# Optimization experiments

Hardware: AMD Instinct MI355X
Metric: run time of the kernel (lower is better)

The kernel has to match this reference:

```python
import jax, jax.numpy as jnp
import numpy as np
from jax.ops import segment_sum

N_NODES = 50000
N_EDGES = 800000
HIDDEN = 96
N_CLASSES = 10
N_GRAPHS = 64


def gcn_conv(x, W, b, src, dst, num_nodes):
    """PyG GCNConv: symmetric-normalized aggregation with self-loops.
    out = D^{-1/2} (A + I) D^{-1/2} (x W) + b, with D the degree of A + I.
    Self-loop contribution handled analytically instead of appending edges.
    """
    ones = jnp.ones((src.shape[0],), dtype=x.dtype)
    deg = segment_sum(ones, dst, num_segments=num_nodes) + 1.0  # +1 for self-loop
    dinv = jax.lax.rsqrt(deg)
    h = x @ W  # [N, H] small GEMM
    norm = dinv[src] * dinv[dst]  # [E]
    msg = h[src] * norm[:, None]  # [E, H] dominant gather
    out = segment_sum(msg, dst, num_segments=num_nodes)  # scatter-add
    out = out + h * (dinv * dinv)[:, None]  # self-loop term
    return out + b


def setup_inputs() -> dict:
    key = jax.random.key(0)
    ks = jax.random.split(key, 12)
    x = jax.random.normal(ks[0], (N_NODES, HIDDEN), dtype=jnp.float32)
    edge_index = jax.random.randint(ks[1], (2, N_EDGES), 0, N_NODES, dtype=jnp.int64)
    batch = jnp.sort(jax.random.randint(ks[2], (N_NODES,), 0, N_GRAPHS, dtype=jnp.int64))
    s = 1.0 / np.sqrt(HIDDEN)
    W0 = jax.random.normal(ks[3], (HIDDEN, HIDDEN), dtype=jnp.float32) * s
    b0 = jnp.zeros((HIDDEN,), dtype=jnp.float32)
    W1 = jax.random.normal(ks[4], (HIDDEN, HIDDEN), dtype=jnp.float32) * s
    b1 = jnp.zeros((HIDDEN,), dtype=jnp.float32)
    W2 = jax.random.normal(ks[5], (HIDDEN, HIDDEN), dtype=jnp.float32) * s
    b2 = jnp.zeros((HIDDEN,), dtype=jnp.float32)
    W_lin = jax.random.normal(ks[6], (HIDDEN, N_CLASSES), dtype=jnp.float32) * s
    b_lin = jnp.zeros((N_CLASSES,), dtype=jnp.float32)
    return {"x": x, "edge_index": edge_index, "batch": batch,
            "W0": W0, "b0": b0, "W1": W1, "b1": b1, "W2": W2, "b2": b2,
            "W_lin": W_lin, "b_lin": b_lin}


def reference(x, edge_index, batch, W0, b0, W1, b1, W2, b2, W_lin, b_lin):
    src, dst = edge_index[0], edge_index[1]
    n = x.shape[0]
    h = jax.nn.relu(gcn_conv(x, W0, b0, src, dst, n))
    h = jax.nn.relu(gcn_conv(h, W1, b1, src, dst, n))
    h = gcn_conv(h, W2, b2, src, dst, n)  # last layer: no activation
    # global_mean_pool over batch index
    sums = segment_sum(h, batch, num_segments=N_GRAPHS)  # [G, H]
    cnts = segment_sum(jnp.ones((n,), dtype=h.dtype), batch, num_segments=N_GRAPHS)
    pooled = sums / jnp.maximum(cnts, 1.0)[:, None]
    # dropout is identity in eval mode
    return pooled @ W_lin + b_lin  # [G, num_classes]
```

## Files before the change

kernel.cpp:

```cpp
#include <hip/hip_runtime.h>
#include <hip/hip_bf16.h>

#define HID 96
#define NGRAPHS 64
#define SENT 0xC3C3u
#define NROWS 50116

typedef __attribute__((ext_vector_type(8))) short short8;
typedef __attribute__((ext_vector_type(4))) float floatx4;
typedef __attribute__((ext_vector_type(2))) float floatx2;
typedef __attribute__((ext_vector_type(8))) unsigned short ushort8v;
typedef __attribute__((ext_vector_type(2))) unsigned int uint2v;

__device__ __forceinline__ unsigned short f32_to_bf16(float f) {
    unsigned int u = __builtin_bit_cast(unsigned int, f);
    u += 0x7fff + ((u >> 16) & 1);
    return (unsigned short)(u >> 16);
}
__device__ __forceinline__ unsigned char f32_to_fp8(float f) {
    return (unsigned char)(__builtin_amdgcn_cvt_pk_fp8_f32(f, f, 0, false) & 0xff);
}
__device__ __forceinline__ void fp8x8_decode(uint2v u, float* __restrict__ o) {
    floatx2 a0 = __builtin_amdgcn_cvt_pk_f32_fp8(u[0], false);
    floatx2 a1 = __builtin_amdgcn_cvt_pk_f32_fp8(u[0], true);
    floatx2 a2 = __builtin_amdgcn_cvt_pk_f32_fp8(u[1], false);
    floatx2 a3 = __builtin_amdgcn_cvt_pk_f32_fp8(u[1], true);
    o[0] = a0[0]; o[1] = a0[1]; o[2] = a1[0]; o[3] = a1[1];
    o[4] = a2[0]; o[5] = a2[1]; o[6] = a3[0]; o[7] = a3[1];
}

__device__ __forceinline__ void gather_core4(
    const unsigned char* __restrict__ h8, const unsigned short* __restrict__ csr,
    int r0, int r1, int r2, int TAIL, int it2, int pe8,
    float* __restrict__ aA, float* __restrict__ aB) {
    int s = r0;
    ushort8v i0 = *(const ushort8v*)(csr + (s < r2 ? s : TAIL));
    ushort8v i1 = *(const ushort8v*)(csr + (s + 8 < r2 ? s + 8 : TAIL));
    for (int it = 0; it < it2; ++it) {
        uint2v v0[8], v1[8];
#pragma unroll
        for (int j = 0; j < 8; ++j)
            v0[j] = *(const uint2v*)(h8 + (int)i0[j] * HID + pe8);
#pragma unroll
        for (int j = 0; j < 8; ++j)
            v1[j] = *(const uint2v*)(h8 + (int)i1[j] * HID + pe8);
        int sn = s + 16;
        ushort8v n0 = *(const ushort8v*)(csr + (sn < r2 ? sn : TAIL));
        ushort8v n1 = *(const ushort8v*)(csr + (sn + 8 < r2 ? sn + 8 : TAIL));
#pragma unroll
        for (int h = 0; h < 4; ++h) {
            float t[8] = {0, 0, 0, 0, 0, 0, 0, 0};
#pragma unroll
            for (int j = 0; j < 4; ++j) {
                float d[8];
                fp8x8_decode((h < 2 ? v0 : v1)[(h & 1) * 4 + j], d);
#pragma unroll
                for (int f = 0; f < 8; ++f) t[f] += d[f];
            }
            int bh = s + h * 4;
            bool bA = bh < r1;
            bool bV = bh < r2;
#pragma unroll
            for (int f = 0; f < 8; ++f) {
                float x = bA ? t[f] : 0.0f;
                float v = bV ? t[f] : 0.0f;
                aA[f] += x;
                aB[f] += v - x;
            }
        }
        i0 = n0;
        i1 = n1;
        s = sn;
    }
}

__global__ __launch_bounds__(256) void init_kernel(
    int* __restrict__ deg, float* __restrict__ psum,
    unsigned char* __restrict__ bufA, unsigned char* __restrict__ bufB, int N,
    int NB, const float* __restrict__ W0, const float* __restrict__ W1,
    const float* __restrict__ W2, unsigned short* __restrict__ Wz) {
    int b = blockIdx.x;
    if (b >= NB) {
        int wsel = b - NB;
        const float* W = (wsel == 0) ? W0 : (wsel == 1) ? W1 : W2;
        unsigned short* dst = Wz + wsel * HID * HID;
        for (int e = threadIdx.x; e < HID * HID; e += blockDim.x) {
            int k = e / HID, n = e % HID;
            int nt = n >> 4, kki = k >> 5, quad = (k >> 3) & 3, j = k & 7;
            int lane = (n & 15) | (quad << 4);
            dst[(((nt * 3 + kki) * 64 + lane) << 3) | j] = f32_to_bf16(W[e]);
        }
        return;
    }
    int i = b * 256 + threadIdx.x;
    if (i < N) deg[i] = 0;
    if (i < NGRAPHS * HID + NGRAPHS) psum[i] = 0.0f;
    if (i < HID) {
        bufA[(size_t)SENT * HID + i] = 0;
        bufB[(size_t)SENT * HID + i] = 0;
    }
}

__global__ void deg_kernel(const int* __restrict__ dst, int* __restrict__ deg,
                           int n_edges) {
    int t = blockIdx.x * blockDim.x + threadIdx.x;
    int e0 = t * 4;
    if (e0 + 4 <= n_edges) {
        int4 d4 = *(const int4*)(dst + e0);
        atomicAdd(&deg[d4.x], 1);
        atomicAdd(&deg[d4.y], 1);
        atomicAdd(&deg[d4.z], 1);
        atomicAdd(&deg[d4.w], 1);
    } else {
        for (int e = e0; e < n_edges; e++) atomicAdd(&deg[dst[e]], 1);
    }
}

__global__ __launch_bounds__(256) void scan_phaseA(const int* __restrict__ deg,
                                                   float* __restrict__ dinv,
                                                   int* __restrict__ blocksum,
                                                   int N) {
    int i = blockIdx.x * 256 + threadIdx.x;
    int d = (i < N) ? deg[i] : 0;
    if (i < N) dinv[i] = rsqrtf((float)d + 1.0f);
    int v = (d + 3) & ~3;
#pragma unroll
    for (int off = 32; off > 0; off >>= 1) v += __shfl_down(v, off, 64);
    __shared__ int s[4];
    if ((threadIdx.x & 63) == 0) s[threadIdx.x >> 6] = v;
    __syncthreads();
    if (threadIdx.x == 0) blocksum[blockIdx.x] = s[0] + s[1] + s[2] + s[3];
}

__global__ __launch_bounds__(256) void scan_phaseC(const int* __restrict__ deg,
                                                   const int* __restrict__ blocksum,
                                                   int* __restrict__ rowptr,
                                                   int* __restrict__ cursor,
                                                   int N, int NB) {
    int t = threadIdx.x;
    int mine = (t < NB && t < blockIdx.x) ? blocksum[t] : 0;
#pragma unroll
    for (int off = 32; off > 0; off >>= 1) mine += __shfl_down(mine, off, 64);
    __shared__ int ps[4];
    if ((t & 63) == 0) ps[t >> 6] = mine;
    __syncthreads();
    int pref = ps[0] + ps[1] + ps[2] + ps[3];

    __shared__ int s[256];
    int i = blockIdx.x * 256 + t;
    int own = (i < N) ? (deg[i] + 3) & ~3 : 0;
    s[t] = own;
    __syncthreads();
#pragma unroll
    for (int off = 1; off < 256; off <<= 1) {
        int v = (t >= off) ? s[t - off] : 0;
        __syncthreads();
        s[t] += v;
        __syncthreads();
    }
    if (i < N) {
        int r = pref + s[t] - own;
        rowptr[i] = r;
        cursor[i] = r;
        if (i == N - 1) rowptr[N] = r + own;
    }
}

__global__ void csr_fill(const int* __restrict__ src, const int* __restrict__ dst,
                         int* __restrict__ cursor,
                         unsigned short* __restrict__ csr_src, int n_edges) {
    int t = blockIdx.x * blockDim.x + threadIdx.x;
    int e0 = t * 8;
    if (e0 + 8 <= n_edges) {
        int4 da = *(const int4*)(dst + e0);
        int4 db = *(const int4*)(dst + e0 + 4);
        int4 sa = *(const int4*)(src + e0);
        int4 sb = *(const int4*)(src + e0 + 4);
        int p0 = atomicAdd(&cursor[da.x], 1);
        int p1 = atomicAdd(&cursor[da.y], 1);
        int p2 = atomicAdd(&cursor[da.z], 1);
        int p3 = atomicAdd(&cursor[da.w], 1);
        int p4 = atomicAdd(&cursor[db.x], 1);
        int p5 = atomicAdd(&cursor[db.y], 1);
        int p6 = atomicAdd(&cursor[db.z], 1);
        int p7 = atomicAdd(&cursor[db.w], 1);
        csr_src[p0] = (unsigned short)sa.x;
        csr_src[p1] = (unsigned short)sa.y;
        csr_src[p2] = (unsigned short)sa.z;
        csr_src[p3] = (unsigned short)sa.w;
        csr_src[p4] = (unsigned short)sb.x;
        csr_src[p5] = (unsigned short)sb.y;
        csr_src[p6] = (unsigned short)sb.z;
        csr_src[p7] = (unsigned short)sb.w;
    } else {
        for (int e = e0; e < n_edges; e++) {
            int p = atomicAdd(&cursor[dst[e]], 1);
            csr_src[p] = (unsigned short)src[e];
        }
    }
}

__global__ __launch_bounds__(256) void gemm0_f32(
    const float* __restrict__ X, const unsigned short* __restrict__ Wz,
    const float* __restrict__ dinv, unsigned char* __restrict__ Out, int Mtiles) {
    int wv = threadIdx.x >> 6;
    int lane = threadIdx.x & 63;
    int quad = lane >> 4;
    int mrow = lane & 15;
    int tt = blockIdx.x * 2 + (wv >> 1);
    int half = wv & 1;
    if (tt >= Mtiles) return;

    short8 bfrag[9];
    const short8* Wz8 = (const short8*)Wz;
#pragma unroll
    for (int f = 0; f < 9; f++) bfrag[f] = Wz8[(half * 9 + f) * 64 + lane];

    int m0 = tt * 16;
    const float* arow = X + (size_t)(m0 + mrow) * HID + quad * 8;
    short8 a[3];
#pragma unroll
    for (int kb = 0; kb < 3; kb++) {
        float4 u = *(const float4*)(arow + kb * 32);
        float4 v = *(const float4*)(arow + kb * 32 + 4);
        short8 t;
        t[0] = (short)f32_to_bf16(u.x); t[1] = (short)f32_to_bf16(u.y);
        t[2] = (short)f32_to_bf16(u.z); t[3] = (short)f32_to_bf16(u.w);
        t[4] = (short)f32_to_bf16(v.x); t[5] = (short)f32_to_bf16(v.y);
        t[6] = (short)f32_to_bf16(v.z); t[7] = (short)f32_to_bf16(v.w);
        a[kb] = t;
    }
    float dscale[4];
#pragma unroll
    for (int r = 0; r < 4; r++) dscale[r] = dinv[m0 + quad * 4 + r];
    unsigned char* orow = Out + (size_t)m0 * HID;
#pragma unroll
    for (int ntl = 0; ntl < 3; ntl++) {
        int nt = half * 3 + ntl;
        floatx4 c = {0.0f, 0.0f, 0.0f, 0.0f};
        c = __builtin_amdgcn_mfma_f32_16x16x32_bf16(a[0], bfrag[ntl * 3 + 0], c, 0, 0, 0);
        c = __builtin_amdgcn_mfma_f32_16x16x32_bf16(a[1], bfrag[ntl * 3 + 1], c, 0, 0, 0);
        c = __builtin_amdgcn_mfma_f32_16x16x32_bf16(a[2], bfrag[ntl * 3 + 2], c, 0, 0, 0);
#pragma unroll
        for (int r = 0; r < 4; r++)
            orow[(size_t)(quad * 4 + r) * HID + nt * 16 + mrow] =
                f32_to_fp8(c[r] * dscale[r]);
    }
}

__global__ __launch_bounds__(256) void fused_gather_gemm(
    const unsigned char* __restrict__ h8, const int* __restrict__ rowptr,
    const unsigned short* __restrict__ csr, const float* __restrict__ dinv,
    const float* __restrict__ bias, const unsigned short* __restrict__ Wz,
    unsigned char* __restrict__ Out, int Mtiles, int N) {
    __shared__ unsigned short tile[2][16][104];
    int wv = threadIdx.x >> 6;
    int lane = threadIdx.x & 63;
    int quad = lane >> 4;
    int mrow = lane & 15;
    int tsel = wv >> 1;
    int half = wv & 1;
    int tt = blockIdx.x * 2 + tsel;
    bool active = tt < Mtiles;
    int g = lane >> 4;
    int p = lane & 15;
    int pe = (p < 12) ? p : 11;
    int pe8 = pe * 8;

    if (active) {
        int TAIL = rowptr[N];
        int j0 = half * 8 + g * 2;
        int na = tt * 16 + j0;
        int r0 = rowptr[na], r1 = rowptr[na + 1], r2 = rowptr[na + 2];
        float da = dinv[na], db = dinv[na + 1];
        float aA[8], aB[8];
        uint2v sva = *(const uint2v*)(h8 + (size_t)na * HID + pe8);
        uint2v svb = *(const uint2v*)(h8 + (size_t)(na + 1) * HID + pe8);
        fp8x8_decode(sva, aA);
        fp8x8_decode(svb, aB);
        int it2 = (r2 - r0 + 15) >> 4;
        int o = __shfl_xor(it2, 16, 64);
        it2 = it2 > o ? it2 : o;
        o = __shfl_xor(it2, 32, 64);
        it2 = it2 > o ? it2 : o;
        gather_core4(h8, csr, r0, r1, r2, TAIL, it2, pe8, aA, aB);
        float4 bb0 = *(const float4*)(bias + pe8);
        float4 bb1 = *(const float4*)(bias + pe8 + 4);
        float bv[8] = {bb0.x, bb0.y, bb0.z, bb0.w, bb1.x, bb1.y, bb1.z, bb1.w};
        if (p < 12) {
            ushort8v oA, oB;
#pragma unroll
            for (int f = 0; f < 8; ++f) {
                oA[f] = f32_to_bf16(fmaxf(aA[f] * da + bv[f], 0.0f));
                oB[f] = f32_to_bf16(fmaxf(aB[f] * db + bv[f], 0.0f));
            }
            *(ushort8v*)(&tile[tsel][j0][pe8]) = oA;
            *(ushort8v*)(&tile[tsel][j0 + 1][pe8]) = oB;
        }
    }
    __syncthreads();
    if (!active) return;

    short8 bfrag[9];
    const short8* Wz8 = (const short8*)Wz;
#pragma unroll
    for (int f = 0; f < 9; f++) bfrag[f] = Wz8[(half * 9 + f) * 64 + lane];

    const unsigned short* tp = &tile[tsel][0][0];
    short8 a[3];
#pragma unroll
    for (int kb = 0; kb < 3; kb++)
        a[kb] = *(const short8*)(tp + mrow * 104 + quad * 8 + kb * 32);
    int n0 = tt * 16;
    float dscale[4];
#pragma unroll
    for (int r = 0; r < 4; r++) dscale[r] = dinv[n0 + quad * 4 + r];
    unsigned char* orow = Out + (size_t)n0 * HID;
#pragma unroll
    for (int ntl = 0; ntl < 3; ntl++) {
        int nt = half * 3 + ntl;
        floatx4 c = {0.0f, 0.0f, 0.0f, 0.0f};
        c = __builtin_amdgcn_mfma_f32_16x16x32_bf16(a[0], bfrag[ntl * 3 + 0], c, 0, 0, 0);
        c = __builtin_amdgcn_mfma_f32_16x16x32_bf16(a[1], bfrag[ntl * 3 + 1], c, 0, 0, 0);
        c = __builtin_amdgcn_mfma_f32_16x16x32_bf16(a[2], bfrag[ntl * 3 + 2], c, 0, 0, 0);
#pragma unroll
        for (int r = 0; r < 4; r++)
            orow[(size_t)(quad * 4 + r) * HID + nt * 16 + mrow] =
                f32_to_fp8(c[r] * dscale[r]);
    }
}

__global__ __launch_bounds__(256) void gather_pool(
    const unsigned char* __restrict__ h8, const int* __restrict__ rowptr,
    const unsigned short* __restrict__ csr, const float* __restrict__ dinv,
    const float* __restrict__ bias, const int* __restrict__ batch,
    float* __restrict__ psum, float* __restrict__ pcnt, int Ntiles8, int N) {
    __shared__ float stage[4][8][96];
    int wv = threadIdx.x >> 6;
    int lane = threadIdx.x & 63;
    int tt = blockIdx.x * 4 + wv;
    bool active = tt < Ntiles8;
    int g = lane >> 4;
    int p = lane & 15;
    int pe = (p < 12) ? p : 11;
    int pe8 = pe * 8;

    if (active) {
        int TAIL = rowptr[N];
        int n0 = tt * 8;
        int na = n0 + g * 2;
        int r0 = rowptr[na], r1 = rowptr[na + 1], r2 = rowptr[na + 2];
        float da = dinv[na], db = dinv[na + 1];
        float aA[8], aB[8];
        uint2v sva = *(const uint2v*)(h8 + (size_t)na * HID + pe8);
        uint2v svb = *(const uint2v*)(h8 + (size_t)(na + 1) * HID + pe8);
        fp8x8_decode(sva, aA);
        fp8x8_decode(svb, aB);
        int it2 = (r2 - r0 + 15) >> 4;
        int o = __shfl_xor(it2, 16, 64);
        it2 = it2 > o ? it2 : o;
        o = __shfl_xor(it2, 32, 64);
        it2 = it2 > o ? it2 : o;
        gather_core4(h8, csr, r0, r1, r2, TAIL, it2, pe8, aA, aB);
        float4 bb0 = *(const float4*)(bias + pe8);
        float4 bb1 = *(const float4*)(bias + pe8 + 4);
        float bv[8] = {bb0.x, bb0.y, bb0.z, bb0.w, bb1.x, bb1.y, bb1.z, bb1.w};
        if (p < 12) {
            floatx4 oa0 = {aA[0] * da + bv[0], aA[1] * da + bv[1],
                           aA[2] * da + bv[2], aA[3] * da + bv[3]};
            floatx4 oa1 = {aA[4] * da + bv[4], aA[5] * da + bv[5],
                           aA[6] * da + bv[6], aA[7] * da + bv[7]};
            floatx4 ob0 = {aB[0] * db + bv[0], aB[1] * db + bv[1],
                           aB[2] * db + bv[2], aB[3] * db + bv[3]};
            floatx4 ob1 = {aB[4] * db + bv[4], aB[5] * db + bv[5],
                           aB[6] * db + bv[6], aB[7] * db + bv[7]};
            *(floatx4*)(&stage[wv][g * 2][pe8]) = oa0;
            *(floatx4*)(&stage[wv][g * 2][pe8 + 4]) = oa1;
            *(floatx4*)(&stage[wv][g * 2 + 1][pe8]) = ob0;
            *(floatx4*)(&stage[wv][g * 2 + 1][pe8 + 4]) = ob1;
        }
    }
    __syncthreads();

    int t = threadIdx.x;
    if (t < 96) {
        int n0b = blockIdx.x * 32;
        int limit = N - n0b;
        if (limit > 32) limit = 32;
        int g_cur = batch[n0b];
        float s = 0.0f;
        int cnt = 0;
        for (int j = 0; j < limit; ++j) {
            int gb = batch[n0b + j];
            if (gb != g_cur) {
                atomicAdd(&psum[g_cur * HID + t], s);
                if (t == 0) atomicAdd(&pcnt[g_cur], (float)cnt);
                s = 0.0f;
                cnt = 0;
                g_cur = gb;
            }
            s += stage[j >> 3][j & 7][t];
            cnt++;
        }
        atomicAdd(&psum[g_cur * HID + t], s);
        if (t == 0) atomicAdd(&pcnt[g_cur], (float)cnt);
    }
}

__global__ __launch_bounds__(640) void final_kernel(
    const float* __restrict__ sums, const float* __restrict__ cnts,
    const float* __restrict__ Wlin, const float* __restrict__ blin,
    float* __restrict__ out) {
    int t = threadIdx.x;
    if (t >= NGRAPHS * 10) return;
    int g = t / 10;
    int c = t % 10;
    float denom = fmaxf(cnts[g], 1.0f);
    float acc = blin[c];
#pragma unroll
    for (int f = 0; f < HID; f++)
        acc += (sums[g * HID + f] / denom) * Wlin[f * 10 + c];
    out[t] = acc;
}

extern "C" void kernel_launch(void* const* d_in, const int* in_sizes, int n_in,
                              void* d_out, int out_size, void* d_ws,
                              size_t ws_size, hipStream_t stream) {
    const float* x = (const float*)d_in[0];
    const int* edge = (const int*)d_in[1];
    const int* batch = (const int*)d_in[2];
    const float* W[3] = {(const float*)d_in[3], (const float*)d_in[5],
                         (const float*)d_in[7]};
    const float* B[3] = {(const float*)d_in[4], (const float*)d_in[6],
                         (const float*)d_in[8]};
    const float* Wlin = (const float*)d_in[9];
    const float* blin = (const float*)d_in[10];
    float* out = (float*)d_out;

    int N = in_sizes[0] / HID;
    int E = in_sizes[1] / 2;
    const int* src = edge;
    const int* dst = edge + E;
    int NB = (N + 255) / 256;

    char* ws = (char*)d_ws;
    size_t off = 0;
    auto alloc = [&](size_t bytes) {
        void* p = ws + off;
        off += (bytes + 255) & ~(size_t)255;
        return p;
    };
    int* deg = (int*)alloc((size_t)N * 4);
    float* dinv = (float*)alloc((size_t)N * 4);
    int* rowptr = (int*)alloc(((size_t)N + 1) * 4);
    int* cursor = (int*)alloc((size_t)N * 4);
    int* blocksum = (int*)alloc((size_t)NB * 4);
    size_t csr_cap = (size_t)E + 4 * (size_t)N;
    unsigned short* csr_src = (unsigned short*)alloc(csr_cap * 2 + 64);
    unsigned short* Wz = (unsigned short*)alloc(3 * HID * HID * 2);
    unsigned char* bufA = (unsigned char*)alloc((size_t)NROWS * HID);
    unsigned char* bufB = (unsigned char*)alloc((size_t)NROWS * HID);
    float* psum = (float*)alloc((NGRAPHS * HID + NGRAPHS) * 4);
    float* pcnt = psum + NGRAPHS * HID;

    hipMemsetAsync(csr_src, 0xC3, csr_cap * 2, stream);
    init_kernel<<<NB + 3, 256, 0, stream>>>(deg, psum, bufA, bufB, N, NB,
                                            W[0], W[1], W[2], Wz);
    deg_kernel<<<(E / 4 + 255) / 256, 256, 0, stream>>>(dst, deg, E);
    scan_phaseA<<<NB, 256, 0, stream>>>(deg, dinv, blocksum, N);
    scan_phaseC<<<NB, 256, 0, stream>>>(deg, blocksum, rowptr, cursor, N, NB);
    csr_fill<<<(E / 8 + 255) / 256, 256, 0, stream>>>(src, dst, cursor, csr_src, E);

    int Mtiles = (N + 15) / 16;
    int grid2 = (Mtiles + 1) / 2;
    int Ntiles8 = (N + 7) / 8;
    int gridp = (Ntiles8 + 3) / 4;

    gemm0_f32<<<grid2, 256, 0, stream>>>(x, Wz, dinv, bufA, Mtiles);
    fused_gather_gemm<<<grid2, 256, 0, stream>>>(
        bufA, rowptr, csr_src, dinv, B[0], Wz + 1 * HID * HID, bufB, Mtiles, N);
    fused_gather_gemm<<<grid2, 256, 0, stream>>>(
        bufB, rowptr, csr_src, dinv, B[1], Wz + 2 * HID * HID, bufA, Mtiles, N);
    gather_pool<<<gridp, 256, 0, stream>>>(bufA, rowptr, csr_src, dinv, B[2],
                                           batch, psum, pcnt, Ntiles8, N);
    final_kernel<<<1, 640, 0, stream>>>(psum, pcnt, Wlin, blin, out);
}
```

Measured before the change: 272.5 us.

## Deepen CSR index prefetch and split pooling atomics across replicated partial buffers

The gather loop now keeps two 16-index groups in flight, loading CSR indices two iterations ahead so the index fetch latency is hidden behind more feature loads. Separately, the mean-pool partial sums are spread over 8 replicated accumulators selected by block index, which reduces atomic contention on the same graph rows. The final kernel reduces the 8 copies in shared memory before the linear layer. This costs extra registers in the gather loop and a slightly larger final reduction. The init zeroing must cover the larger buffer, which relies on enough init blocks.

```diff
diff --git a/kernel.cpp b/kernel.cpp
--- a/kernel.cpp
+++ b/kernel.cpp
@@ -5,6 +5,7 @@
 #define NGRAPHS 64
 #define SENT 0xC3C3u
 #define NROWS 50116
+#define NSPLIT 8
 
 typedef __attribute__((ext_vector_type(8))) short short8;
 typedef __attribute__((ext_vector_type(4))) float floatx4;
@@ -34,19 +35,21 @@
     int r0, int r1, int r2, int TAIL, int it2, int pe8,
     float* __restrict__ aA, float* __restrict__ aB) {
     int s = r0;
-    ushort8v i0 = *(const ushort8v*)(csr + (s < r2 ? s : TAIL));
-    ushort8v i1 = *(const ushort8v*)(csr + (s + 8 < r2 ? s + 8 : TAIL));
+    ushort8v ia0 = *(const ushort8v*)(csr + (s      < r2 ? s      : TAIL));
+    ushort8v ia1 = *(const ushort8v*)(csr + (s + 8  < r2 ? s + 8  : TAIL));
+    ushort8v ib0 = *(const ushort8v*)(csr + (s + 16 < r2 ? s + 16 : TAIL));
+    ushort8v ib1 = *(const ushort8v*)(csr + (s + 24 < r2 ? s + 24 : TAIL));
     for (int it = 0; it < it2; ++it) {
         uint2v v0[8], v1[8];
 #pragma unroll
         for (int j = 0; j < 8; ++j)
-            v0[j] = *(const uint2v*)(h8 + (int)i0[j] * HID + pe8);
+            v0[j] = *(const uint2v*)(h8 + (int)ia0[j] * HID + pe8);
 #pragma unroll
         for (int j = 0; j < 8; ++j)
-            v1[j] = *(const uint2v*)(h8 + (int)i1[j] * HID + pe8);
-        int sn = s + 16;
-        ushort8v n0 = *(const ushort8v*)(csr + (sn < r2 ? sn : TAIL));
-        ushort8v n1 = *(const ushort8v*)(csr + (sn + 8 < r2 ? sn + 8 : TAIL));
+            v1[j] = *(const uint2v*)(h8 + (int)ia1[j] * HID + pe8);
+        int sp = s + 32;
+        ushort8v n0 = *(const ushort8v*)(csr + (sp     < r2 ? sp     : TAIL));
+        ushort8v n1 = *(const ushort8v*)(csr + (sp + 8 < r2 ? sp + 8 : TAIL));
 #pragma unroll
         for (int h = 0; h < 4; ++h) {
             float t[8] = {0, 0, 0, 0, 0, 0, 0, 0};
@@ -68,9 +71,11 @@
                 aB[f] += v - x;
             }
         }
-        i0 = n0;
-        i1 = n1;
-        s = sn;
+        ia0 = ib0;
+        ia1 = ib1;
+        ib0 = n0;
+        ib1 = n1;
+        s += 16;
     }
 }
 
@@ -94,7 +99,7 @@
     }
     int i = b * 256 + threadIdx.x;
     if (i < N) deg[i] = 0;
-    if (i < NGRAPHS * HID + NGRAPHS) psum[i] = 0.0f;
+    if (i < NSPLIT * (NGRAPHS * HID + NGRAPHS)) psum[i] = 0.0f;
     if (i < HID) {
         bufA[(size_t)SENT * HID + i] = 0;
         bufB[(size_t)SENT * HID + i] = 0;
@@ -384,6 +389,8 @@
 
     int t = threadIdx.x;
     if (t < 96) {
+        float* pbase = psum + (size_t)(blockIdx.x & (NSPLIT - 1)) * (NGRAPHS * HID);
+        float* pcbase = pcnt + (size_t)(blockIdx.x & (NSPLIT - 1)) * NGRAPHS;
         int n0b = blockIdx.x * 32;
         int limit = N - n0b;
         if (limit > 32) limit = 32;
@@ -393,8 +400,8 @@
         for (int j = 0; j < limit; ++j) {
             int gb = batch[n0b + j];
             if (gb != g_cur) {
-                atomicAdd(&psum[g_cur * HID + t], s);
-                if (t == 0) atomicAdd(&pcnt[g_cur], (float)cnt);
+                atomicAdd(&pbase[g_cur * HID + t], s);
+                if (t == 0) atomicAdd(&pcbase[g_cur], (float)cnt);
                 s = 0.0f;
                 cnt = 0;
                 g_cur = gb;
@@ -402,8 +409,8 @@
             s += stage[j >> 3][j & 7][t];
             cnt++;
         }
-        atomicAdd(&psum[g_cur * HID + t], s);
-        if (t == 0) atomicAdd(&pcnt[g_cur], (float)cnt);
+        atomicAdd(&pbase[g_cur * HID + t], s);
+        if (t == 0) atomicAdd(&pcbase[g_cur], (float)cnt);
     }
 }
 
@@ -411,15 +418,30 @@
     const float* __restrict__ sums, const float* __restrict__ cnts,
     const float* __restrict__ Wlin, const float* __restrict__ blin,
     float* __restrict__ out) {
+    __shared__ float rs[NGRAPHS * HID];
+    __shared__ float rc[NGRAPHS];
     int t = threadIdx.x;
+    for (int i = t; i < NGRAPHS * HID; i += 640) {
+        float s = 0.0f;
+#pragma unroll
+        for (int k = 0; k < NSPLIT; ++k) s += sums[(size_t)k * NGRAPHS * HID + i];
+        rs[i] = s;
+    }
+    if (t < NGRAPHS) {
+        float s = 0.0f;
+#pragma unroll
+        for (int k = 0; k < NSPLIT; ++k) s += cnts[(size_t)k * NGRAPHS + t];
+        rc[t] = s;
+    }
+    __syncthreads();
     if (t >= NGRAPHS * 10) return;
     int g = t / 10;
     int c = t % 10;
-    float denom = fmaxf(cnts[g], 1.0f);
+    float denom = fmaxf(rc[g], 1.0f);
     float acc = blin[c];
 #pragma unroll
     for (int f = 0; f < HID; f++)
-        acc += (sums[g * HID + f] / denom) * Wlin[f * 10 + c];
+        acc += (rs[g * HID + f] / denom) * Wlin[f * 10 + c];
     out[t] = acc;
 }
 
@@ -460,8 +482,8 @@
     unsigned short* Wz = (unsigned short*)alloc(3 * HID * HID * 2);
     unsigned char* bufA = (unsigned char*)alloc((size_t)NROWS * HID);
     unsigned char* bufB = (unsigned char*)alloc((size_t)NROWS * HID);
-    float* psum = (float*)alloc((NGRAPHS * HID + NGRAPHS) * 4);
-    float* pcnt = psum + NGRAPHS * HID;
+    float* psum = (float*)alloc((size_t)NSPLIT * (NGRAPHS * HID + NGRAPHS) * 4);
+    float* pcnt = psum + (size_t)NSPLIT * NGRAPHS * HID;
 
     hipMemsetAsync(csr_src, 0xC3, csr_cap * 2, stream);
     init_kernel<<<NB + 3, 256, 0, stream>>>(deg, psum, bufA, bufB, N, NB,
```

Result: no change. 271.2 us (median of 2 runs) (-0.5%).
